# Kernel optimization log

Hardware: AMD Instinct MI355X
Metric: run time of the kernel (lower is better)

## Reference

```python
import jax, jax.numpy as jnp
import numpy as np

NUM_HEADS = 4
SPATIAL_DS = 2
EPS = 1e-5


def setup_inputs() -> dict:
    key = jax.random.key(0)
    ks = jax.random.split(key, 6)
    B, C, H, W = 8, 256, 64, 64
    hd = C // NUM_HEADS
    return {
        "x": jax.random.normal(ks[0], (B, C, H, W), jnp.float32),
        "gn_w": jnp.ones((C,), jnp.float32),
        "gn_b": jnp.zeros((C,), jnp.float32),
        "wq": jax.random.normal(ks[1], (C, C), jnp.float32) * (C ** -0.5),
        "wk": jax.random.normal(ks[2], (hd, C), jnp.float32) * (C ** -0.5),
        "wv": jax.random.normal(ks[3], (hd, C), jnp.float32) * (C ** -0.5),
        "wo": jax.random.normal(ks[4], (C, C), jnp.float32) * (C ** -0.5),
        "gamma": jnp.full((C,), 1e-4, jnp.float32),
    }


def reference(x, gn_w, gn_b, wq, wk, wv, wo, gamma):
    B, C, H, W = x.shape
    hd = C // NUM_HEADS
    scale = hd ** -0.5
    ds = SPATIAL_DS

    # GroupNorm with 1 group: normalize over (C,H,W) per sample, per-channel affine
    mu = jnp.mean(x, axis=(1, 2, 3), keepdims=True)
    var = jnp.var(x, axis=(1, 2, 3), keepdims=True)
    xn = (x - mu) * jax.lax.rsqrt(var + EPS)
    xn = xn * gn_w[None, :, None, None] + gn_b[None, :, None, None]

    # Q projection (1x1 conv == channel matmul): (B, heads, N, hd)
    q = jnp.einsum('oc,bchw->bohw', wq, xn).reshape(B, NUM_HEADS, hd, H * W)
    q = jnp.swapaxes(q, 2, 3)  # (B, h, N, hd)

    # AvgPool2d(ds, ds) on normalized input for K/V
    Hd, Wd = H // ds, W // ds
    x_ds = xn.reshape(B, C, Hd, ds, Wd, ds).mean(axis=(3, 5))

    k = jnp.einsum('oc,bchw->bohw', wk, x_ds).reshape(B, hd, Hd * Wd)
    k = jnp.swapaxes(k, 1, 2)  # (B, M, hd) single shared head
    v = jnp.einsum('oc,bchw->bohw', wv, x_ds).reshape(B, hd, Hd * Wd)
    v = jnp.swapaxes(v, 1, 2)  # (B, M, hd)

    # Multi-query attention: queries per-head, shared K/V
    attn = jnp.einsum('bhnd,bmd->bhnm', q, k) * scale
    attn = jax.nn.softmax(attn, axis=-1)
    out = jnp.einsum('bhnm,bmd->bhnd', attn, v)  # (B, h, N, hd)

    out = jnp.swapaxes(out, 2, 3).reshape(B, C, H, W)
    out = jnp.einsum('oc,bchw->bohw', wo, out)

    return x + out * gamma[None, :, None, None]
```

## Files before the change

kernel.cpp:

```cpp
#include <hip/hip_runtime.h>


#define CNT_INV (1.0f/1048576.0f)
#define EPSV 1e-5f
#define QSCALE 0.18033688f

#define WS_STATS 0
#define WS_XNT   64
#define WS_XDS   4194368
#define WS_Q     5242944
#define WS_K     9437248
#define WS_V     9699392
#define WS_AOT   9961536
#define WS_WQB   14155840
#define WS_WKV   14188608
#define WS_WOB   14204992

typedef __attribute__((ext_vector_type(8))) short bf8_t;
typedef __attribute__((ext_vector_type(4))) float f4_t;

static __device__ __forceinline__ unsigned fbits(float f) {
  union { float f; unsigned u; } v; v.f = f; return v.u;
}
static __device__ __forceinline__ unsigned short f2bf(float f) {
  unsigned u = fbits(f);
  return (unsigned short)((u + 0x7fffu + ((u >> 16) & 1u)) >> 16);
}
static __device__ __forceinline__ unsigned pk_rnd(float a, float b) {
  return __builtin_amdgcn_perm(fbits(b) + 0x8000u, fbits(a) + 0x8000u, 0x07060302u);
}
static __device__ __forceinline__ unsigned pk_tr(float a, float b) {
  return __builtin_amdgcn_perm(fbits(b), fbits(a), 0x07060302u);
}
static __device__ __forceinline__ float bf2f(unsigned short h) {
  union { unsigned u; float f; } v; v.u = ((unsigned)h) << 16; return v.f;
}
static __device__ __forceinline__ float fexp2(float x) {
  float r; asm("v_exp_f32 %0, %1" : "=v"(r) : "v"(x)); return r;
}

__global__ __launch_bounds__(256) void k_prep_stats(const float* __restrict__ x,
                                                    const float* __restrict__ wq,
                                                    const float* __restrict__ wk,
                                                    const float* __restrict__ wv,
                                                    const float* __restrict__ wo,
                                                    float* __restrict__ stats,
                                                    unsigned short* __restrict__ wqb,
                                                    unsigned short* __restrict__ wkvb,
                                                    unsigned short* __restrict__ wob) {
  const int blk = blockIdx.x;
  const int t = threadIdx.x;
  if (blk < 512) {
    const int b = blk >> 6;
    const int chunk = blk & 63;
    const float4* xb = (const float4*)(x + (size_t)b * 1048576 + (size_t)chunk * 16384);
    float s = 0.f, s2 = 0.f;
#pragma unroll
    for (int it = 0; it < 16; ++it) {
      float4 v = xb[it * 256 + t];
      s  += v.x + v.y + v.z + v.w;
      s2 += v.x * v.x + v.y * v.y + v.z * v.z + v.w * v.w;
    }
#pragma unroll
    for (int o = 32; o > 0; o >>= 1) {
      s  += __shfl_down(s, o);
      s2 += __shfl_down(s2, o);
    }
    __shared__ float red[8];
    const int wid = t >> 6;
    if ((t & 63) == 0) { red[wid] = s; red[4 + wid] = s2; }
    __syncthreads();
    if (t == 0) {
      atomicAdd(&stats[b * 2 + 0], red[0] + red[1] + red[2] + red[3]);
      atomicAdd(&stats[b * 2 + 1], red[4] + red[5] + red[6] + red[7]);
    }
  } else {
    const int idx = (blk - 512) * 256 + t;
    if (idx < 65536) wqb[idx] = f2bf(wq[idx]);
    else if (idx < 81920) wkvb[idx - 65536] = f2bf(wk[idx - 65536]);
    else if (idx < 98304) wkvb[idx - 65536] = f2bf(wv[idx - 81920]);
    else if (idx < 163840) wob[idx - 98304] = f2bf(wo[idx - 98304]);
  }
}

__global__ __launch_bounds__(256) void k_xnt(const float* __restrict__ x,
                                             const float* __restrict__ gnw,
                                             const float* __restrict__ gnb,
                                             const float* __restrict__ stats,
                                             unsigned short* __restrict__ xnT,
                                             unsigned short* __restrict__ xdsT) {
  __shared__ unsigned short T[128][72];
  const int t = threadIdx.x;
  const int b = blockIdx.z, c0 = blockIdx.y * 64, hp = blockIdx.x;
  const int n0 = hp * 128;
  const float mu = stats[b * 2 + 0] * CNT_INV;
  const float rstd = rsqrtf(stats[b * 2 + 1] * CNT_INV - mu * mu + EPSV);
  const int n4 = (t & 31) * 4, cl = t >> 5;
#pragma unroll
  for (int p = 0; p < 8; ++p) {
    const int c = c0 + p * 8 + cl;
    const float gw = gnw[c] * rstd;
    const float gb = gnb[c] - mu * rstd * gnw[c];
    float4 v = *(const float4*)&x[(size_t)(b * 256 + c) * 4096 + n0 + n4];
    T[n4 + 0][p * 8 + cl] = f2bf(v.x * gw + gb);
    T[n4 + 1][p * 8 + cl] = f2bf(v.y * gw + gb);
    T[n4 + 2][p * 8 + cl] = f2bf(v.z * gw + gb);
    T[n4 + 3][p * 8 + cl] = f2bf(v.w * gw + gb);
  }
  __syncthreads();
  {
    const int r = t >> 1, ch = (t & 1) * 32;
    unsigned short* dst = xnT + ((size_t)b * 4096 + n0 + r) * 256 + c0 + ch;
#pragma unroll
    for (int u = 0; u < 4; ++u)
      *(uint4*)(dst + u * 8) = *(const uint4*)&T[r][ch + u * 8];
  }
  {
    const int wd = t & 31, c8 = (t >> 5) * 8;
    uint4 u0 = *(const uint4*)&T[2 * wd][c8];
    uint4 u1 = *(const uint4*)&T[2 * wd + 1][c8];
    uint4 u2 = *(const uint4*)&T[64 + 2 * wd][c8];
    uint4 u3 = *(const uint4*)&T[64 + 2 * wd + 1][c8];
    const unsigned* p0 = (const unsigned*)&u0; const unsigned* p1 = (const unsigned*)&u1;
    const unsigned* p2 = (const unsigned*)&u2; const unsigned* p3 = (const unsigned*)&u3;
    unsigned outp[4];
#pragma unroll
    for (int i = 0; i < 4; ++i) {
      float lo = (bf2f((unsigned short)p0[i]) + bf2f((unsigned short)p1[i]) +
                  bf2f((unsigned short)p2[i]) + bf2f((unsigned short)p3[i])) * 0.25f;
      float hi = (bf2f((unsigned short)(p0[i] >> 16)) + bf2f((unsigned short)(p1[i] >> 16)) +
                  bf2f((unsigned short)(p2[i] >> 16)) + bf2f((unsigned short)(p3[i] >> 16))) * 0.25f;
      outp[i] = pk_rnd(lo, hi);
    }
    *(uint4*)(xdsT + ((size_t)b * 1024 + hp * 32 + wd) * 256 + c0 + c8) = *(uint4*)outp;
  }
}

__global__ __launch_bounds__(256) void k_gemm_q(const unsigned short* __restrict__ wqb,
                                                const unsigned short* __restrict__ xnT,
                                                unsigned short* __restrict__ qbf) {
  const int t = threadIdx.x;
  const int h = t >> 6, l = t & 63, lane16 = l & 15, quad = l >> 4;
  const int n0 = blockIdx.x * 64, b = blockIdx.y;
  const unsigned short* Abase = wqb + (size_t)(h * 64 + lane16) * 256 + quad * 8;
  const unsigned short* Bbase = xnT + ((size_t)b * 4096 + n0 + lane16) * 256 + quad * 8;
  f4_t acc[4][4];
#pragma unroll
  for (int i = 0; i < 4; ++i)
#pragma unroll
    for (int j = 0; j < 4; ++j) acc[i][j] = (f4_t){0.f, 0.f, 0.f, 0.f};
  bf8_t Ac[4], Bc[4];
#pragma unroll
  for (int og = 0; og < 4; ++og) Ac[og] = *(const bf8_t*)(Abase + (size_t)og * 16 * 256);
#pragma unroll
  for (int ng = 0; ng < 4; ++ng) Bc[ng] = *(const bf8_t*)(Bbase + (size_t)ng * 16 * 256);
  for (int kc = 0; kc < 256; kc += 32) {
    const int kn = (kc + 32) & 255;
    bf8_t An[4], Bn[4];
#pragma unroll
    for (int og = 0; og < 4; ++og) An[og] = *(const bf8_t*)(Abase + (size_t)og * 16 * 256 + kn);
#pragma unroll
    for (int ng = 0; ng < 4; ++ng) Bn[ng] = *(const bf8_t*)(Bbase + (size_t)ng * 16 * 256 + kn);
#pragma unroll
    for (int og = 0; og < 4; ++og)
#pragma unroll
      for (int ng = 0; ng < 4; ++ng)
        acc[og][ng] = __builtin_amdgcn_mfma_f32_16x16x32_bf16(Ac[og], Bc[ng], acc[og][ng], 0, 0, 0);
#pragma unroll
    for (int og = 0; og < 4; ++og) Ac[og] = An[og];
#pragma unroll
    for (int ng = 0; ng < 4; ++ng) Bc[ng] = Bn[ng];
  }
#pragma unroll
  for (int og = 0; og < 4; ++og)
#pragma unroll
    for (int ng = 0; ng < 4; ++ng) {
      const int n = n0 + ng * 16 + lane16;
      uint2 p;
      p.x = pk_rnd(acc[og][ng][0] * QSCALE, acc[og][ng][1] * QSCALE);
      p.y = pk_rnd(acc[og][ng][2] * QSCALE, acc[og][ng][3] * QSCALE);
      *(uint2*)(qbf + ((size_t)(b * 4 + h) * 4096 + n) * 64 + og * 16 + quad * 4) = p;
    }
}

__global__ __launch_bounds__(256) void k_gemm_kv(const unsigned short* __restrict__ wkvb,
                                                 const unsigned short* __restrict__ xdsT,
                                                 unsigned short* __restrict__ kbf,
                                                 unsigned short* __restrict__ vtbf) {
  const int t = threadIdx.x;
  const int w = t >> 6, l = t & 63, lane16 = l & 15, quad = l >> 4;
  const int m0 = blockIdx.x * 64, b = blockIdx.y;
  const unsigned short* Abase = wkvb + (size_t)(w * 32 + lane16) * 256 + quad * 8;
  const unsigned short* Bbase = xdsT + ((size_t)b * 1024 + m0 + lane16) * 256 + quad * 8;
  f4_t acc[2][4];
#pragma unroll
  for (int i = 0; i < 2; ++i)
#pragma unroll
    for (int j = 0; j < 4; ++j) acc[i][j] = (f4_t){0.f, 0.f, 0.f, 0.f};
  bf8_t Ac[2], Bc[4];
#pragma unroll
  for (int og = 0; og < 2; ++og) Ac[og] = *(const bf8_t*)(Abase + (size_t)og * 16 * 256);
#pragma unroll
  for (int mg = 0; mg < 4; ++mg) Bc[mg] = *(const bf8_t*)(Bbase + (size_t)mg * 16 * 256);
  for (int kc = 0; kc < 256; kc += 32) {
    const int kn = (kc + 32) & 255;
    bf8_t An[2], Bn[4];
#pragma unroll
    for (int og = 0; og < 2; ++og) An[og] = *(const bf8_t*)(Abase + (size_t)og * 16 * 256 + kn);
#pragma unroll
    for (int mg = 0; mg < 4; ++mg) Bn[mg] = *(const bf8_t*)(Bbase + (size_t)mg * 16 * 256 + kn);
#pragma unroll
    for (int og = 0; og < 2; ++og)
#pragma unroll
      for (int mg = 0; mg < 4; ++mg)
        acc[og][mg] = __builtin_amdgcn_mfma_f32_16x16x32_bf16(Ac[og], Bc[mg], acc[og][mg], 0, 0, 0);
#pragma unroll
    for (int og = 0; og < 2; ++og) Ac[og] = An[og];
#pragma unroll
    for (int mg = 0; mg < 4; ++mg) Bc[mg] = Bn[mg];
  }
  if (w < 2) {
#pragma unroll
    for (int og = 0; og < 2; ++og)
#pragma unroll
      for (int mg = 0; mg < 4; ++mg) {
        const int m = m0 + mg * 16 + lane16;
        uint2 p;
        p.x = pk_rnd(acc[og][mg][0], acc[og][mg][1]);
        p.y = pk_rnd(acc[og][mg][2], acc[og][mg][3]);
        *(uint2*)(kbf + (size_t)b * 65536 + (size_t)m * 64 + w * 32 + og * 16 + quad * 4) = p;
      }
  } else {
#pragma unroll
    for (int og = 0; og < 2; ++og)
#pragma unroll
      for (int mg = 0; mg < 4; ++mg) {
        const int m = m0 + mg * 16 + lane16;
        const int d0 = (w - 2) * 32 + og * 16 + quad * 4;
#pragma unroll
        for (int r = 0; r < 4; ++r)
          vtbf[(size_t)b * 65536 + (size_t)(d0 + r) * 1024 + m] = f2bf(acc[og][mg][r]);
      }
  }
}

__global__ __launch_bounds__(128) void k_attn_mfma(const unsigned short* __restrict__ qbf,
                                                   const unsigned short* __restrict__ kbf,
                                                   const unsigned short* __restrict__ vtbf,
                                                   unsigned short* __restrict__ aoT) {
  __shared__ __align__(16) unsigned short plds[2][2][64][36];
  const int t = threadIdx.x;
  const int w = t >> 6, l = t & 63, lane16 = l & 15, quad = l >> 4;
  const int h = blockIdx.y, b = blockIdx.z;
  const int q0 = blockIdx.x * 128 + w * 64;

  const unsigned short* qb = qbf + ((size_t)(b * 4 + h) * 4096 + q0) * 64;
  const unsigned short* kb = kbf + (size_t)b * 65536;
  const unsigned short* vb = vtbf + (size_t)b * 65536;

  bf8_t Qf[4][2];
#pragma unroll
  for (int qg = 0; qg < 4; ++qg)
#pragma unroll
    for (int dc = 0; dc < 2; ++dc)
      Qf[qg][dc] = *(const bf8_t*)(qb + (qg * 16 + lane16) * 64 + dc * 32 + quad * 8);

  f4_t O[4][4];
#pragma unroll
  for (int dg = 0; dg < 4; ++dg)
#pragma unroll
    for (int qg = 0; qg < 4; ++qg) O[dg][qg] = (f4_t){0.f, 0.f, 0.f, 0.f};
  float den[4] = {0.f, 0.f, 0.f, 0.f};

#define SSTEP(KREG, BUF)                                                      \
  {                                                                           \
    _Pragma("unroll")                                                         \
    for (int qg = 0; qg < 4; ++qg) {                                          \
      _Pragma("unroll")                                                       \
      for (int s = 0; s < 2; ++s) {                                           \
        f4_t S = (f4_t){0.f, 0.f, 0.f, 0.f};                                  \
        S = __builtin_amdgcn_mfma_f32_16x16x32_bf16(KREG[s][0], Qf[qg][0], S, 0, 0, 0); \
        S = __builtin_amdgcn_mfma_f32_16x16x32_bf16(KREG[s][1], Qf[qg][1], S, 0, 0, 0); \
        float e0 = fexp2(S[0]);                                               \
        float e1 = fexp2(S[1]);                                               \
        float e2 = fexp2(S[2]);                                               \
        float e3 = fexp2(S[3]);                                               \
        den[qg] += (e0 + e1) + (e2 + e3);                                     \
        uint2 p; p.x = pk_tr(e0, e1); p.y = pk_tr(e2, e3);                    \
        *(uint2*)&plds[w][BUF][qg * 16 + lane16][s * 16 + quad * 4] = p;      \
      }                                                                       \
    }                                                                         \
  }

  bf8_t Kc[2][2];
#pragma unroll
  for (int s = 0; s < 2; ++s)
#pragma unroll
    for (int dc = 0; dc < 2; ++dc)
      Kc[s][dc] = *(const bf8_t*)(kb + (size_t)(s * 16 + lane16) * 64 + dc * 32 + quad * 8);
  SSTEP(Kc, 0);

  bf8_t Vc[4];
#pragma unroll
  for (int s = 0; s < 2; ++s)
#pragma unroll
    for (int dc = 0; dc < 2; ++dc)
      Kc[s][dc] = *(const bf8_t*)(kb + (size_t)(32 + s * 16 + lane16) * 64 + dc * 32 + quad * 8);
#pragma unroll
  for (int dg = 0; dg < 4; ++dg)
    Vc[dg] = *(const bf8_t*)(vb + (size_t)(dg * 16 + lane16) * 1024 + quad * 8);

  for (int it = 1; it < 32; ++it) {
    const int cb = it & 1, pb = cb ^ 1;
    bf8_t Pf[4];
#pragma unroll
    for (int qg = 0; qg < 4; ++qg)
      Pf[qg] = *(const bf8_t*)&plds[w][pb][qg * 16 + lane16][quad * 8];
    const int kvk = ((it + 1) & 31) * 32;
    const int kvv = it * 32;
    bf8_t K2[2][2], V2[4];
#pragma unroll
    for (int s = 0; s < 2; ++s)
#pragma unroll
      for (int dc = 0; dc < 2; ++dc)
        K2[s][dc] = *(const bf8_t*)(kb + (size_t)(kvk + s * 16 + lane16) * 64 + dc * 32 + quad * 8);
#pragma unroll
    for (int dg = 0; dg < 4; ++dg)
      V2[dg] = *(const bf8_t*)(vb + (size_t)(dg * 16 + lane16) * 1024 + kvv + quad * 8);
#pragma unroll
    for (int dg = 0; dg < 4; ++dg)
#pragma unroll
      for (int qg = 0; qg < 4; ++qg)
        O[dg][qg] = __builtin_amdgcn_mfma_f32_16x16x32_bf16(Vc[dg], Pf[qg], O[dg][qg], 0, 0, 0);
    SSTEP(Kc, cb);
#pragma unroll
    for (int s = 0; s < 2; ++s)
#pragma unroll
      for (int dc = 0; dc < 2; ++dc) Kc[s][dc] = K2[s][dc];
#pragma unroll
    for (int dg = 0; dg < 4; ++dg) Vc[dg] = V2[dg];
  }
  {
    bf8_t Pf[4];
#pragma unroll
    for (int qg = 0; qg < 4; ++qg)
      Pf[qg] = *(const bf8_t*)&plds[w][1][qg * 16 + lane16][quad * 8];
#pragma unroll
    for (int dg = 0; dg < 4; ++dg)
#pragma unroll
      for (int qg = 0; qg < 4; ++qg)
        O[dg][qg] = __builtin_amdgcn_mfma_f32_16x16x32_bf16(Vc[dg], Pf[qg], O[dg][qg], 0, 0, 0);
  }

  float rden[4];
#pragma unroll
  for (int qg = 0; qg < 4; ++qg) {
    float d = den[qg];
    d += __shfl_xor(d, 16);
    d += __shfl_xor(d, 32);
    rden[qg] = 1.f / d;
  }

#pragma unroll
  for (int dg = 0; dg < 4; ++dg)
#pragma unroll
    for (int qg = 0; qg < 4; ++qg) {
      const int c0 = h * 64 + dg * 16 + quad * 4;
      const int n = q0 + qg * 16 + lane16;
      uint2 p;
      p.x = pk_rnd(O[dg][qg][0] * rden[qg], O[dg][qg][1] * rden[qg]);
      p.y = pk_rnd(O[dg][qg][2] * rden[qg], O[dg][qg][3] * rden[qg]);
      *(uint2*)(aoT + ((size_t)b * 4096 + n) * 256 + c0) = p;
    }
#undef SSTEP
}

__global__ __launch_bounds__(256) void k_gemm_wo(const unsigned short* __restrict__ wob,
                                                 const unsigned short* __restrict__ aoT,
                                                 const float* __restrict__ x,
                                                 const float* __restrict__ gamma,
                                                 float* __restrict__ outp) {
  const int t = threadIdx.x;
  const int w = t >> 6, l = t & 63, lane16 = l & 15, quad = l >> 4;
  const int n0 = blockIdx.x * 64, b = blockIdx.y;
  const unsigned short* Abase = wob + (size_t)(w * 64 + lane16) * 256 + quad * 8;
  const unsigned short* Bbase = aoT + ((size_t)b * 4096 + n0 + lane16) * 256 + quad * 8;
  f4_t acc[4][4];
#pragma unroll
  for (int i = 0; i < 4; ++i)
#pragma unroll
    for (int j = 0; j < 4; ++j) acc[i][j] = (f4_t){0.f, 0.f, 0.f, 0.f};
  bf8_t Ac[4], Bc[4];
#pragma unroll
  for (int og = 0; og < 4; ++og) Ac[og] = *(const bf8_t*)(Abase + (size_t)og * 16 * 256);
#pragma unroll
  for (int ng = 0; ng < 4; ++ng) Bc[ng] = *(const bf8_t*)(Bbase + (size_t)ng * 16 * 256);
  for (int kc = 0; kc < 256; kc += 32) {
    const int kn = (kc + 32) & 255;
    bf8_t An[4], Bn[4];
#pragma unroll
    for (int og = 0; og < 4; ++og) An[og] = *(const bf8_t*)(Abase + (size_t)og * 16 * 256 + kn);
#pragma unroll
    for (int ng = 0; ng < 4; ++ng) Bn[ng] = *(const bf8_t*)(Bbase + (size_t)ng * 16 * 256 + kn);
#pragma unroll
    for (int og = 0; og < 4; ++og)
#pragma unroll
      for (int ng = 0; ng < 4; ++ng)
        acc[og][ng] = __builtin_amdgcn_mfma_f32_16x16x32_bf16(Ac[og], Bc[ng], acc[og][ng], 0, 0, 0);
#pragma unroll
    for (int og = 0; og < 4; ++og) Ac[og] = An[og];
#pragma unroll
    for (int ng = 0; ng < 4; ++ng) Bc[ng] = Bn[ng];
  }
#pragma unroll
  for (int og = 0; og < 4; ++og) {
    float4 g4 = *(const float4*)&gamma[w * 64 + og * 16 + quad * 4];
    const float g[4] = {g4.x, g4.y, g4.z, g4.w};
#pragma unroll
    for (int ng = 0; ng < 4; ++ng) {
      const int n = n0 + ng * 16 + lane16;
#pragma unroll
      for (int r = 0; r < 4; ++r) {
        const int o = w * 64 + og * 16 + quad * 4 + r;
        const size_t ix = ((size_t)(b * 256 + o)) * 4096 + n;
        outp[ix] = x[ix] + g[r] * acc[og][ng][r];
      }
    }
  }
}

extern "C" void kernel_launch(void* const* d_in, const int* in_sizes, int n_in,
                              void* d_out, int out_size, void* d_ws, size_t ws_size,
                              hipStream_t stream) {
  const float* x     = (const float*)d_in[0];
  const float* gnw   = (const float*)d_in[1];
  const float* gnb   = (const float*)d_in[2];
  const float* wq    = (const float*)d_in[3];
  const float* wk    = (const float*)d_in[4];
  const float* wv    = (const float*)d_in[5];
  const float* wo    = (const float*)d_in[6];
  const float* gamma = (const float*)d_in[7];
  float* out = (float*)d_out;
  float* ws  = (float*)d_ws;
  unsigned short* xnT  = (unsigned short*)(ws + WS_XNT);
  unsigned short* xdsT = (unsigned short*)(ws + WS_XDS);
  unsigned short* qbf  = (unsigned short*)(ws + WS_Q);
  unsigned short* kbf  = (unsigned short*)(ws + WS_K);
  unsigned short* vtbf = (unsigned short*)(ws + WS_V);
  unsigned short* aoT  = (unsigned short*)(ws + WS_AOT);
  unsigned short* wqb  = (unsigned short*)(ws + WS_WQB);
  unsigned short* wkvb = (unsigned short*)(ws + WS_WKV);
  unsigned short* wob  = (unsigned short*)(ws + WS_WOB);

  hipMemsetAsync(ws, 0, 256, stream);
  k_prep_stats<<<1152, 256, 0, stream>>>(x, wq, wk, wv, wo, ws + WS_STATS, wqb, wkvb, wob);
  k_xnt<<<dim3(32, 4, 8), 256, 0, stream>>>(x, gnw, gnb, ws + WS_STATS, xnT, xdsT);
  k_gemm_q<<<dim3(64, 8), 256, 0, stream>>>(wqb, xnT, qbf);
  k_gemm_kv<<<dim3(16, 8), 256, 0, stream>>>(wkvb, xdsT, kbf, vtbf);
  k_attn_mfma<<<dim3(32, 4, 8), 128, 0, stream>>>(qbf, kbf, vtbf, aoT);
  k_gemm_wo<<<dim3(64, 8), 256, 0, stream>>>(wob, aoT, x, gamma, out);
}
```

Measured before the change: 232.7 us.

## Fuse Q projection, attention and output projection into one kernel

Replaces the separate Q GEMM, attention and Wo GEMM kernels with one fused kernel per 64-query tile that computes Q into shared memory, runs attention per head in each wave, stages the attention output in shared memory and applies the output projection with the residual. This removes the global round trips for Q and the attention output and two launches. In exchange, each block handles all heads for fewer queries, so there are fewer, larger blocks with more LDS and register pressure, and the GEMM loops drop their software prefetch.

```diff
diff --git a/kernel.cpp b/kernel.cpp
--- a/kernel.cpp
+++ b/kernel.cpp
@@ -8,13 +8,11 @@
 #define WS_STATS 0
 #define WS_XNT   64
 #define WS_XDS   4194368
-#define WS_Q     5242944
-#define WS_K     9437248
-#define WS_V     9699392
-#define WS_AOT   9961536
-#define WS_WQB   14155840
-#define WS_WKV   14188608
-#define WS_WOB   14204992
+#define WS_K     5242944
+#define WS_V     5505088
+#define WS_WQB   5767232
+#define WS_WKV   5800000
+#define WS_WOB   5816384
 
 typedef __attribute__((ext_vector_type(8))) short bf8_t;
 typedef __attribute__((ext_vector_type(4))) float f4_t;
@@ -136,53 +134,6 @@
   }
 }
 
-__global__ __launch_bounds__(256) void k_gemm_q(const unsigned short* __restrict__ wqb,
-                                                const unsigned short* __restrict__ xnT,
-                                                unsigned short* __restrict__ qbf) {
-  const int t = threadIdx.x;
-  const int h = t >> 6, l = t & 63, lane16 = l & 15, quad = l >> 4;
-  const int n0 = blockIdx.x * 64, b = blockIdx.y;
-  const unsigned short* Abase = wqb + (size_t)(h * 64 + lane16) * 256 + quad * 8;
-  const unsigned short* Bbase = xnT + ((size_t)b * 4096 + n0 + lane16) * 256 + quad * 8;
-  f4_t acc[4][4];
-#pragma unroll
-  for (int i = 0; i < 4; ++i)
-#pragma unroll
-    for (int j = 0; j < 4; ++j) acc[i][j] = (f4_t){0.f, 0.f, 0.f, 0.f};
-  bf8_t Ac[4], Bc[4];
-#pragma unroll
-  for (int og = 0; og < 4; ++og) Ac[og] = *(const bf8_t*)(Abase + (size_t)og * 16 * 256);
-#pragma unroll
-  for (int ng = 0; ng < 4; ++ng) Bc[ng] = *(const bf8_t*)(Bbase + (size_t)ng * 16 * 256);
-  for (int kc = 0; kc < 256; kc += 32) {
-    const int kn = (kc + 32) & 255;
-    bf8_t An[4], Bn[4];
-#pragma unroll
-    for (int og = 0; og < 4; ++og) An[og] = *(const bf8_t*)(Abase + (size_t)og * 16 * 256 + kn);
-#pragma unroll
-    for (int ng = 0; ng < 4; ++ng) Bn[ng] = *(const bf8_t*)(Bbase + (size_t)ng * 16 * 256 + kn);
-#pragma unroll
-    for (int og = 0; og < 4; ++og)
-#pragma unroll
-      for (int ng = 0; ng < 4; ++ng)
-        acc[og][ng] = __builtin_amdgcn_mfma_f32_16x16x32_bf16(Ac[og], Bc[ng], acc[og][ng], 0, 0, 0);
-#pragma unroll
-    for (int og = 0; og < 4; ++og) Ac[og] = An[og];
-#pragma unroll
-    for (int ng = 0; ng < 4; ++ng) Bc[ng] = Bn[ng];
-  }
-#pragma unroll
-  for (int og = 0; og < 4; ++og)
-#pragma unroll
-    for (int ng = 0; ng < 4; ++ng) {
-      const int n = n0 + ng * 16 + lane16;
-      uint2 p;
-      p.x = pk_rnd(acc[og][ng][0] * QSCALE, acc[og][ng][1] * QSCALE);
-      p.y = pk_rnd(acc[og][ng][2] * QSCALE, acc[og][ng][3] * QSCALE);
-      *(uint2*)(qbf + ((size_t)(b * 4 + h) * 4096 + n) * 64 + og * 16 + quad * 4) = p;
-    }
-}
-
 __global__ __launch_bounds__(256) void k_gemm_kv(const unsigned short* __restrict__ wkvb,
                                                  const unsigned short* __restrict__ xdsT,
                                                  unsigned short* __restrict__ kbf,
@@ -244,26 +195,63 @@
   }
 }
 
-__global__ __launch_bounds__(128) void k_attn_mfma(const unsigned short* __restrict__ qbf,
-                                                   const unsigned short* __restrict__ kbf,
-                                                   const unsigned short* __restrict__ vtbf,
-                                                   unsigned short* __restrict__ aoT) {
-  __shared__ __align__(16) unsigned short plds[2][2][64][36];
+__global__ __launch_bounds__(256) void k_fused(const unsigned short* __restrict__ wqb,
+                                               const unsigned short* __restrict__ xnT,
+                                               const unsigned short* __restrict__ kbf,
+                                               const unsigned short* __restrict__ vtbf,
+                                               const unsigned short* __restrict__ wob,
+                                               const float* __restrict__ x,
+                                               const float* __restrict__ gamma,
+                                               float* __restrict__ outp) {
+  __shared__ __align__(16) unsigned short smem[20480];
   const int t = threadIdx.x;
   const int w = t >> 6, l = t & 63, lane16 = l & 15, quad = l >> 4;
-  const int h = blockIdx.y, b = blockIdx.z;
-  const int q0 = blockIdx.x * 128 + w * 64;
-
-  const unsigned short* qb = qbf + ((size_t)(b * 4 + h) * 4096 + q0) * 64;
+  const int n0 = blockIdx.x * 64, b = blockIdx.y;
+  const int h = w;
+  unsigned short* qst = smem + w * 4608;
+  unsigned short (*plds)[64][40] = (unsigned short (*)[64][40])(smem + w * 5120);
+  unsigned short (*aos)[264] = (unsigned short (*)[264])smem;
+
   const unsigned short* kb = kbf + (size_t)b * 65536;
   const unsigned short* vb = vtbf + (size_t)b * 65536;
 
+  {
+    const unsigned short* Abase = wqb + (size_t)(h * 64 + lane16) * 256 + quad * 8;
+    const unsigned short* Bbase = xnT + ((size_t)b * 4096 + n0 + lane16) * 256 + quad * 8;
+    f4_t qacc[4][4];
+#pragma unroll
+    for (int i = 0; i < 4; ++i)
+#pragma unroll
+      for (int j = 0; j < 4; ++j) qacc[i][j] = (f4_t){0.f, 0.f, 0.f, 0.f};
+    for (int kc = 0; kc < 256; kc += 32) {
+      bf8_t A[4], Bf[4];
+#pragma unroll
+      for (int og = 0; og < 4; ++og) A[og] = *(const bf8_t*)(Abase + (size_t)og * 16 * 256 + kc);
+#pragma unroll
+      for (int ng = 0; ng < 4; ++ng) Bf[ng] = *(const bf8_t*)(Bbase + (size_t)ng * 16 * 256 + kc);
+#pragma unroll
+      for (int og = 0; og < 4; ++og)
+#pragma unroll
+        for (int ng = 0; ng < 4; ++ng)
+          qacc[og][ng] = __builtin_amdgcn_mfma_f32_16x16x32_bf16(A[og], Bf[ng], qacc[og][ng], 0, 0, 0);
+    }
+#pragma unroll
+    for (int og = 0; og < 4; ++og)
+#pragma unroll
+      for (int ng = 0; ng < 4; ++ng) {
+        uint2 p;
+        p.x = pk_rnd(qacc[og][ng][0] * QSCALE, qacc[og][ng][1] * QSCALE);
+        p.y = pk_rnd(qacc[og][ng][2] * QSCALE, qacc[og][ng][3] * QSCALE);
+        *(uint2*)&qst[(ng * 16 + lane16) * 72 + og * 16 + quad * 4] = p;
+      }
+  }
   bf8_t Qf[4][2];
 #pragma unroll
   for (int qg = 0; qg < 4; ++qg)
 #pragma unroll
     for (int dc = 0; dc < 2; ++dc)
-      Qf[qg][dc] = *(const bf8_t*)(qb + (qg * 16 + lane16) * 64 + dc * 32 + quad * 8);
+      Qf[qg][dc] = *(const bf8_t*)&qst[(qg * 16 + lane16) * 72 + dc * 32 + quad * 8];
+  __syncthreads();
 
   f4_t O[4][4];
 #pragma unroll
@@ -287,7 +275,7 @@
         float e3 = fexp2(S[3]);                                               \
         den[qg] += (e0 + e1) + (e2 + e3);                                     \
         uint2 p; p.x = pk_tr(e0, e1); p.y = pk_tr(e2, e3);                    \
-        *(uint2*)&plds[w][BUF][qg * 16 + lane16][s * 16 + quad * 4] = p;      \
+        *(uint2*)&plds[BUF][qg * 16 + lane16][s * 16 + quad * 4] = p;         \
       }                                                                       \
     }                                                                         \
   }
@@ -315,7 +303,7 @@
     bf8_t Pf[4];
 #pragma unroll
     for (int qg = 0; qg < 4; ++qg)
-      Pf[qg] = *(const bf8_t*)&plds[w][pb][qg * 16 + lane16][quad * 8];
+      Pf[qg] = *(const bf8_t*)&plds[pb][qg * 16 + lane16][quad * 8];
     const int kvk = ((it + 1) & 31) * 32;
     const int kvv = it * 32;
     bf8_t K2[2][2], V2[4];
@@ -344,13 +332,14 @@
     bf8_t Pf[4];
 #pragma unroll
     for (int qg = 0; qg < 4; ++qg)
-      Pf[qg] = *(const bf8_t*)&plds[w][1][qg * 16 + lane16][quad * 8];
+      Pf[qg] = *(const bf8_t*)&plds[1][qg * 16 + lane16][quad * 8];
 #pragma unroll
     for (int dg = 0; dg < 4; ++dg)
 #pragma unroll
       for (int qg = 0; qg < 4; ++qg)
         O[dg][qg] = __builtin_amdgcn_mfma_f32_16x16x32_bf16(Vc[dg], Pf[qg], O[dg][qg], 0, 0, 0);
   }
+#undef SSTEP
 
   float rden[4];
 #pragma unroll
@@ -361,69 +350,51 @@
     rden[qg] = 1.f / d;
   }
 
+  __syncthreads();
 #pragma unroll
   for (int dg = 0; dg < 4; ++dg)
 #pragma unroll
     for (int qg = 0; qg < 4; ++qg) {
       const int c0 = h * 64 + dg * 16 + quad * 4;
-      const int n = q0 + qg * 16 + lane16;
       uint2 p;
       p.x = pk_rnd(O[dg][qg][0] * rden[qg], O[dg][qg][1] * rden[qg]);
       p.y = pk_rnd(O[dg][qg][2] * rden[qg], O[dg][qg][3] * rden[qg]);
-      *(uint2*)(aoT + ((size_t)b * 4096 + n) * 256 + c0) = p;
-    }
-#undef SSTEP
-}
-
-__global__ __launch_bounds__(256) void k_gemm_wo(const unsigned short* __restrict__ wob,
-                                                 const unsigned short* __restrict__ aoT,
-                                                 const float* __restrict__ x,
-                                                 const float* __restrict__ gamma,
-                                                 float* __restrict__ outp) {
-  const int t = threadIdx.x;
-  const int w = t >> 6, l = t & 63, lane16 = l & 15, quad = l >> 4;
-  const int n0 = blockIdx.x * 64, b = blockIdx.y;
-  const unsigned short* Abase = wob + (size_t)(w * 64 + lane16) * 256 + quad * 8;
-  const unsigned short* Bbase = aoT + ((size_t)b * 4096 + n0 + lane16) * 256 + quad * 8;
-  f4_t acc[4][4];
-#pragma unroll
-  for (int i = 0; i < 4; ++i)
-#pragma unroll
-    for (int j = 0; j < 4; ++j) acc[i][j] = (f4_t){0.f, 0.f, 0.f, 0.f};
-  bf8_t Ac[4], Bc[4];
-#pragma unroll
-  for (int og = 0; og < 4; ++og) Ac[og] = *(const bf8_t*)(Abase + (size_t)og * 16 * 256);
-#pragma unroll
-  for (int ng = 0; ng < 4; ++ng) Bc[ng] = *(const bf8_t*)(Bbase + (size_t)ng * 16 * 256);
-  for (int kc = 0; kc < 256; kc += 32) {
-    const int kn = (kc + 32) & 255;
-    bf8_t An[4], Bn[4];
-#pragma unroll
-    for (int og = 0; og < 4; ++og) An[og] = *(const bf8_t*)(Abase + (size_t)og * 16 * 256 + kn);
-#pragma unroll
-    for (int ng = 0; ng < 4; ++ng) Bn[ng] = *(const bf8_t*)(Bbase + (size_t)ng * 16 * 256 + kn);
-#pragma unroll
-    for (int og = 0; og < 4; ++og)
-#pragma unroll
-      for (int ng = 0; ng < 4; ++ng)
-        acc[og][ng] = __builtin_amdgcn_mfma_f32_16x16x32_bf16(Ac[og], Bc[ng], acc[og][ng], 0, 0, 0);
-#pragma unroll
-    for (int og = 0; og < 4; ++og) Ac[og] = An[og];
-#pragma unroll
-    for (int ng = 0; ng < 4; ++ng) Bc[ng] = Bn[ng];
-  }
-#pragma unroll
-  for (int og = 0; og < 4; ++og) {
-    float4 g4 = *(const float4*)&gamma[w * 64 + og * 16 + quad * 4];
-    const float g[4] = {g4.x, g4.y, g4.z, g4.w};
-#pragma unroll
-    for (int ng = 0; ng < 4; ++ng) {
-      const int n = n0 + ng * 16 + lane16;
-#pragma unroll
-      for (int r = 0; r < 4; ++r) {
-        const int o = w * 64 + og * 16 + quad * 4 + r;
-        const size_t ix = ((size_t)(b * 256 + o)) * 4096 + n;
-        outp[ix] = x[ix] + g[r] * acc[og][ng][r];
+      *(uint2*)&aos[qg * 16 + lane16][c0] = p;
+    }
+  __syncthreads();
+
+  {
+    const unsigned short* Wbase = wob + (size_t)(w * 64 + lane16) * 256 + quad * 8;
+    f4_t acc[4][4];
+#pragma unroll
+    for (int i = 0; i < 4; ++i)
+#pragma unroll
+      for (int j = 0; j < 4; ++j) acc[i][j] = (f4_t){0.f, 0.f, 0.f, 0.f};
+    for (int kc = 0; kc < 256; kc += 32) {
+      bf8_t A[4], Bf[4];
+#pragma unroll
+      for (int og = 0; og < 4; ++og) A[og] = *(const bf8_t*)(Wbase + (size_t)og * 16 * 256 + kc);
+#pragma unroll
+      for (int ng = 0; ng < 4; ++ng) Bf[ng] = *(const bf8_t*)&aos[ng * 16 + lane16][kc + quad * 8];
+#pragma unroll
+      for (int og = 0; og < 4; ++og)
+#pragma unroll
+        for (int ng = 0; ng < 4; ++ng)
+          acc[og][ng] = __builtin_amdgcn_mfma_f32_16x16x32_bf16(A[og], Bf[ng], acc[og][ng], 0, 0, 0);
+    }
+#pragma unroll
+    for (int og = 0; og < 4; ++og) {
+      float4 g4 = *(const float4*)&gamma[w * 64 + og * 16 + quad * 4];
+      const float g[4] = {g4.x, g4.y, g4.z, g4.w};
+#pragma unroll
+      for (int ng = 0; ng < 4; ++ng) {
+        const int n = n0 + ng * 16 + lane16;
+#pragma unroll
+        for (int r = 0; r < 4; ++r) {
+          const int o = w * 64 + og * 16 + quad * 4 + r;
+          const size_t ix = ((size_t)(b * 256 + o)) * 4096 + n;
+          outp[ix] = x[ix] + g[r] * acc[og][ng][r];
+        }
       }
     }
   }
@@ -444,10 +415,8 @@
   float* ws  = (float*)d_ws;
   unsigned short* xnT  = (unsigned short*)(ws + WS_XNT);
   unsigned short* xdsT = (unsigned short*)(ws + WS_XDS);
-  unsigned short* qbf  = (unsigned short*)(ws + WS_Q);
   unsigned short* kbf  = (unsigned short*)(ws + WS_K);
   unsigned short* vtbf = (unsigned short*)(ws + WS_V);
-  unsigned short* aoT  = (unsigned short*)(ws + WS_AOT);
   unsigned short* wqb  = (unsigned short*)(ws + WS_WQB);
   unsigned short* wkvb = (unsigned short*)(ws + WS_WKV);
   unsigned short* wob  = (unsigned short*)(ws + WS_WOB);
@@ -455,8 +424,6 @@
   hipMemsetAsync(ws, 0, 256, stream);
   k_prep_stats<<<1152, 256, 0, stream>>>(x, wq, wk, wv, wo, ws + WS_STATS, wqb, wkvb, wob);
   k_xnt<<<dim3(32, 4, 8), 256, 0, stream>>>(x, gnw, gnb, ws + WS_STATS, xnT, xdsT);
-  k_gemm_q<<<dim3(64, 8), 256, 0, stream>>>(wqb, xnT, qbf);
   k_gemm_kv<<<dim3(16, 8), 256, 0, stream>>>(wkvb, xdsT, kbf, vtbf);
-  k_attn_mfma<<<dim3(32, 4, 8), 128, 0, stream>>>(qbf, kbf, vtbf, aoT);
-  k_gemm_wo<<<dim3(64, 8), 256, 0, stream>>>(wob, aoT, x, gamma, out);
-}
+  k_fused<<<dim3(64, 8), 256, 0, stream>>>(wqb, xnT, kbf, vtbf, wob, x, gamma, out);
+}
```

Result: faster. 215.1 us (-7.5%).
